# Kernel optimization log

Measured on AMD Instinct MI355X. Metric: run time of the kernel, lower is better.

## Reference

```python
import jax, jax.numpy as jnp
import numpy as np
import math

D_MODEL = 1024
NHEAD = 16
D_K = D_MODEL // NHEAD
NUM_LAYERS = 4
D_FF = 4096
SEQ = 2048
BATCH = 1
EPS = 1e-5


def _layer_norm(x, g, b):
    mu = jnp.mean(x, axis=-1, keepdims=True)
    var = jnp.mean((x - mu) ** 2, axis=-1, keepdims=True)
    return (x - mu) * jax.lax.rsqrt(var + EPS) * g + b


def setup_inputs() -> dict:
    key = jax.random.key(0)
    ks = jax.random.split(key, 16)
    s = 0.02
    L, D, F = NUM_LAYERS, D_MODEL, D_FF
    inp = {
        "x": jax.random.normal(ks[0], (BATCH, SEQ, D), dtype=jnp.float32),
        "wq": jax.random.normal(ks[1], (L, D, D), dtype=jnp.float32) * s,
        "bq": jnp.zeros((L, D), dtype=jnp.float32),
        "wk": jax.random.normal(ks[2], (L, D, D), dtype=jnp.float32) * s,
        "bk": jnp.zeros((L, D), dtype=jnp.float32),
        "wv": jax.random.normal(ks[3], (L, D, D), dtype=jnp.float32) * s,
        "bv": jnp.zeros((L, D), dtype=jnp.float32),
        "wo": jax.random.normal(ks[4], (L, D, D), dtype=jnp.float32) * s,
        "bo": jnp.zeros((L, D), dtype=jnp.float32),
        "w1": jax.random.normal(ks[5], (L, D, F), dtype=jnp.float32) * s,
        "b1": jnp.zeros((L, F), dtype=jnp.float32),
        "w2": jax.random.normal(ks[6], (L, F, D), dtype=jnp.float32) * s,
        "b2": jnp.zeros((L, D), dtype=jnp.float32),
        "ln1_g": jnp.ones((L, D), dtype=jnp.float32),
        "ln1_b": jnp.zeros((L, D), dtype=jnp.float32),
        "ln2_g": jnp.ones((L, D), dtype=jnp.float32),
        "ln2_b": jnp.zeros((L, D), dtype=jnp.float32),
    }
    return inp


def _transformer(x, wq, bq, wk, bk, wv, bv, wo, bo, w1, b1, w2, b2,
                 ln1_g, ln1_b, ln2_g, ln2_b):
    B, S, D = x.shape
    scale = math.sqrt(D_K)
    for l in range(NUM_LAYERS):
        # multi-head self-attention (manual QKV matmul + softmax + matmul)
        q = (x @ wq[l] + bq[l]).reshape(B, S, NHEAD, D_K).transpose(0, 2, 1, 3)
        k = (x @ wk[l] + bk[l]).reshape(B, S, NHEAD, D_K).transpose(0, 2, 1, 3)
        v = (x @ wv[l] + bv[l]).reshape(B, S, NHEAD, D_K).transpose(0, 2, 1, 3)
        scores = jnp.einsum('bhqd,bhkd->bhqk', q, k) / scale  # [B,H,S,S]
        attn = jax.nn.softmax(scores, axis=-1)
        ctx = jnp.einsum('bhqk,bhkd->bhqd', attn, v)
        ctx = ctx.transpose(0, 2, 1, 3).reshape(B, S, D)
        attn_out = ctx @ wo[l] + bo[l]
        x = _layer_norm(x + attn_out, ln1_g[l], ln1_b[l])
        # feed-forward network with gelu
        h = jax.nn.gelu(x @ w1[l] + b1[l])
        ffn_out = h @ w2[l] + b2[l]
        x = _layer_norm(x + ffn_out, ln2_g[l], ln2_b[l])
    return x


def reference(x, wq, bq, wk, bk, wv, bv, wo, bo, w1, b1, w2, b2,
              ln1_g, ln1_b, ln2_g, ln2_b):
    return _transformer(x, wq, bq, wk, bk, wv, bv, wo, bo, w1, b1, w2, b2,
                        ln1_g, ln1_b, ln2_g, ln2_b)
```

## Files before the change

### kernel.cpp

```cpp
#include <hip/hip_runtime.h>
#include <hip/hip_bf16.h>
#include <math.h>

typedef __hip_bfloat16 bf16;
typedef __attribute__((ext_vector_type(8))) short bf16x8;
typedef __attribute__((ext_vector_type(4))) float f32x4;

#define EPI_NONE 0
#define EPI_BIAS_BF16 1
#define EPI_BIAS_GELU_BF16 2

__device__ __forceinline__ void gload16(const void* g, void* l) {
  __builtin_amdgcn_global_load_lds((const __attribute__((address_space(1))) void*)g,
                                   (__attribute__((address_space(3))) void*)l, 16, 0, 0);
}

__device__ __forceinline__ float gelu_tanh(float x) {
  const float c = 0.7978845608028654f;
  float t = tanhf(c * (x + 0.044715f * x * x * x));
  return 0.5f * x * (1.0f + t);
}

template<int BM, int BN, int EPI, typename CT>
__global__ __launch_bounds__(256) void gemm_bt(
    const bf16* __restrict__ A, long sAz, int lda,
    const bf16* __restrict__ Bt, long sBz, int ldb,
    CT* __restrict__ C, long sCz, int ldc,
    const float* __restrict__ bias,
    int K, float scale)
{
  constexpr int BK = 32;
  constexpr int WM = BM / 2, WN = BN / 2;
  constexpr int MI = WM / 16, NJ = WN / 16;
  constexpr int NA = (BM * BK * 2) / 4096;
  constexpr int NB = (BN * BK * 2) / 4096;
  __shared__ __align__(16) bf16 As[BM * BK];
  __shared__ __align__(16) bf16 Bs[BN * BK];
  const int t = threadIdx.x;
  const int lane = t & 63, w = t >> 6;
  const int wm = (w >> 1) * WM, wn = (w & 1) * WN;
  const int quad = lane >> 4, r16 = lane & 15;
  const long z = blockIdx.z;
  const bf16* Ab = A + z * sAz + (long)blockIdx.y * BM * lda;
  const bf16* Bb = Bt + z * sBz + (long)blockIdx.x * BN * ldb;

  f32x4 acc[MI][NJ];
  #pragma unroll
  for (int i = 0; i < MI; ++i)
    #pragma unroll
    for (int j = 0; j < NJ; ++j)
      acc[i][j] = (f32x4){0.f, 0.f, 0.f, 0.f};

  for (int k0 = 0; k0 < K; k0 += BK) {
    __syncthreads();
    #pragma unroll
    for (int s = 0; s < NA; ++s) {
      int Lb = s * 4096 + t * 16;
      int row = Lb >> 6, colb = Lb & 63;
      gload16((const char*)Ab + (long)row * (lda * 2) + k0 * 2 + colb, (char*)As + Lb);
    }
    #pragma unroll
    for (int s = 0; s < NB; ++s) {
      int Lb = s * 4096 + t * 16;
      int row = Lb >> 6, colb = Lb & 63;
      gload16((const char*)Bb + (long)row * (ldb * 2) + k0 * 2 + colb, (char*)Bs + Lb);
    }
    __syncthreads();

    bf16x8 af[MI], bfv[NJ];
    #pragma unroll
    for (int i = 0; i < MI; ++i)
      af[i] = *(const bf16x8*)&As[(wm + i * 16 + r16) * BK + quad * 8];
    #pragma unroll
    for (int j = 0; j < NJ; ++j)
      bfv[j] = *(const bf16x8*)&Bs[(wn + j * 16 + r16) * BK + quad * 8];
    #pragma unroll
    for (int i = 0; i < MI; ++i)
      #pragma unroll
      for (int j = 0; j < NJ; ++j)
        acc[i][j] = __builtin_amdgcn_mfma_f32_16x16x32_bf16(af[i], bfv[j], acc[i][j], 0, 0, 0);
  }

  CT* Cb = C + z * sCz;
  #pragma unroll
  for (int i = 0; i < MI; ++i) {
    #pragma unroll
    for (int j = 0; j < NJ; ++j) {
      int col = blockIdx.x * BN + wn + j * 16 + r16;
      float bvv = 0.f;
      if constexpr (EPI == EPI_BIAS_BF16 || EPI == EPI_BIAS_GELU_BF16)
        bvv = bias[col];
      #pragma unroll
      for (int r = 0; r < 4; ++r) {
        long row = (long)blockIdx.y * BM + wm + i * 16 + quad * 4 + r;
        float val = acc[i][j][r] * scale + bvv;
        if constexpr (EPI == EPI_BIAS_GELU_BF16) val = gelu_tanh(val);
        if constexpr (sizeof(CT) == 2)
          Cb[row * (long)ldc + col] = __float2bfloat16(val);
        else
          Cb[row * (long)ldc + col] = val;
      }
    }
  }
}

__global__ __launch_bounds__(256) void flash_attn(
    const bf16* __restrict__ qkv, const bf16* __restrict__ vT,
    bf16* __restrict__ ctx)
{
  constexpr int SEQ = 2048, LDP = 72;
  __shared__ __align__(16) bf16 Qs[64 * 64];
  __shared__ __align__(16) bf16 Ks[64 * LDP];
  __shared__ __align__(16) bf16 VTs[64 * LDP];
  __shared__ __align__(16) bf16 Ps[64 * LDP];

  const int t = threadIdx.x;
  const int lane = t & 63, w = t >> 6;
  const int quad = lane >> 4, r16 = lane & 15;
  const int wq0 = w * 16;
  const int s0 = blockIdx.x * 64;
  const int h = blockIdx.y;

  #pragma unroll
  for (int s = 0; s < 2; ++s) {
    int Lb = s * 4096 + t * 16;
    int row = Lb >> 7, colb = Lb & 127;
    int4 v = *(const int4*)(qkv + (long)(s0 + row) * 3072 + h * 64 + (colb >> 1));
    *(int4*)((char*)Qs + Lb) = v;
  }

  const bf16* kp[2]; const bf16* vp[2];
  int krow[2], kcolb[2];
  #pragma unroll
  for (int s = 0; s < 2; ++s) {
    int Lb = s * 4096 + t * 16;
    krow[s] = Lb >> 7; kcolb[s] = Lb & 127;
    kp[s] = qkv + 1024 + (long)h * 64 + (long)krow[s] * 3072 + (kcolb[s] >> 1);
    vp[s] = vT + (long)(h * 64 + krow[s]) * SEQ + (kcolb[s] >> 1);
  }

  int4 rk[2], rv[2];
  #pragma unroll
  for (int s = 0; s < 2; ++s) {
    rk[s] = *(const int4*)(kp[s]);
    rv[s] = *(const int4*)(vp[s]);
  }

  __syncthreads();
  bf16x8 af_q[2];
  #pragma unroll
  for (int kk = 0; kk < 2; ++kk)
    af_q[kk] = *(const bf16x8*)&Qs[(wq0 + r16) * 64 + kk * 32 + quad * 8];

  f32x4 O[4];
  float m_s[4], l_s[4];
  #pragma unroll
  for (int jd = 0; jd < 4; ++jd) O[jd] = (f32x4){0.f, 0.f, 0.f, 0.f};
  #pragma unroll
  for (int r = 0; r < 4; ++r) { m_s[r] = -1e30f; l_s[r] = 0.f; }

  for (int kt = 0; kt < SEQ / 64; ++kt) {
    __syncthreads();
    #pragma unroll
    for (int s = 0; s < 2; ++s) {
      *(int4*)((char*)Ks + (krow[s] * LDP * 2) + kcolb[s]) = rk[s];
      *(int4*)((char*)VTs + (krow[s] * LDP * 2) + kcolb[s]) = rv[s];
    }
    __syncthreads();

    if (kt + 1 < SEQ / 64) {
      long k0n = (long)(kt + 1) * 64;
      #pragma unroll
      for (int s = 0; s < 2; ++s) {
        rk[s] = *(const int4*)(kp[s] + k0n * 3072);
        rv[s] = *(const int4*)(vp[s] + k0n);
      }
    }

    f32x4 sc[4];
    #pragma unroll
    for (int j = 0; j < 4; ++j) sc[j] = (f32x4){0.f, 0.f, 0.f, 0.f};
    #pragma unroll
    for (int kk = 0; kk < 2; ++kk) {
      bf16x8 bk_f[4];
      #pragma unroll
      for (int j = 0; j < 4; ++j)
        bk_f[j] = *(const bf16x8*)&Ks[(j * 16 + r16) * LDP + kk * 32 + quad * 8];
      #pragma unroll
      for (int j = 0; j < 4; ++j)
        sc[j] = __builtin_amdgcn_mfma_f32_16x16x32_bf16(af_q[kk], bk_f[j], sc[j], 0, 0, 0);
    }

    #pragma unroll
    for (int r = 0; r < 4; ++r) {
      float mx = -1e30f;
      #pragma unroll
      for (int j = 0; j < 4; ++j) {
        sc[j][r] *= 0.125f;
        mx = fmaxf(mx, sc[j][r]);
      }
      #pragma unroll
      for (int msk = 1; msk < 16; msk <<= 1)
        mx = fmaxf(mx, __shfl_xor(mx, msk));
      float m_new = fmaxf(m_s[r], mx);
      float alpha = __expf(m_s[r] - m_new);
      m_s[r] = m_new;
      float rs = 0.f;
      #pragma unroll
      for (int j = 0; j < 4; ++j) {
        float pv = __expf(sc[j][r] - m_new);
        sc[j][r] = pv;
        rs += pv;
      }
      #pragma unroll
      for (int msk = 1; msk < 16; msk <<= 1)
        rs += __shfl_xor(rs, msk);
      l_s[r] = l_s[r] * alpha + rs;
      #pragma unroll
      for (int jd = 0; jd < 4; ++jd) O[jd][r] *= alpha;
    }

    {
      int prow = wq0 + quad * 4;
      #pragma unroll
      for (int j = 0; j < 4; ++j)
        #pragma unroll
        for (int r = 0; r < 4; ++r)
          Ps[(prow + r) * LDP + j * 16 + r16] = __float2bfloat16(sc[j][r]);
    }
    __syncthreads();

    #pragma unroll
    for (int kk = 0; kk < 2; ++kk) {
      bf16x8 af_p, bv_f[4];
      af_p = *(const bf16x8*)&Ps[(wq0 + r16) * LDP + kk * 32 + quad * 8];
      #pragma unroll
      for (int jd = 0; jd < 4; ++jd)
        bv_f[jd] = *(const bf16x8*)&VTs[(jd * 16 + r16) * LDP + kk * 32 + quad * 8];
      #pragma unroll
      for (int jd = 0; jd < 4; ++jd)
        O[jd] = __builtin_amdgcn_mfma_f32_16x16x32_bf16(af_p, bv_f[jd], O[jd], 0, 0, 0);
    }
  }

  #pragma unroll
  for (int r = 0; r < 4; ++r) {
    long row = s0 + wq0 + quad * 4 + r;
    float inv = 1.f / l_s[r];
    #pragma unroll
    for (int jd = 0; jd < 4; ++jd)
      ctx[row * 1024 + h * 64 + jd * 16 + r16] = __float2bfloat16(O[jd][r] * inv);
  }
}

__global__ __launch_bounds__(256) void transpose_cast(
    const float* __restrict__ in, bf16* __restrict__ out, int R, int C)
{
  __shared__ bf16 tile[32][33];
  const int tx = threadIdx.x, ty = threadIdx.y;
  const int r0 = blockIdx.y * 32, c0 = blockIdx.x * 32;
  #pragma unroll
  for (int d = 0; d < 32; d += 8)
    tile[ty + d][tx] = __float2bfloat16(in[(long)(r0 + ty + d) * C + c0 + tx]);
  __syncthreads();
  #pragma unroll
  for (int d = 0; d < 32; d += 8)
    out[(long)(c0 + ty + d) * R + r0 + tx] = tile[tx][ty + d];
}

__global__ __launch_bounds__(256) void transpose_bf16(
    const bf16* __restrict__ in, bf16* __restrict__ out, int R, int C, int ldin)
{
  __shared__ bf16 tile[32][33];
  const int tx = threadIdx.x, ty = threadIdx.y;
  const int r0 = blockIdx.y * 32, c0 = blockIdx.x * 32;
  #pragma unroll
  for (int d = 0; d < 32; d += 8)
    tile[ty + d][tx] = in[(long)(r0 + ty + d) * ldin + c0 + tx];
  __syncthreads();
  #pragma unroll
  for (int d = 0; d < 32; d += 8)
    out[(long)(c0 + ty + d) * R + r0 + tx] = tile[tx][ty + d];
}

__device__ __forceinline__ float blk_sum(float v, float* sh) {
  #pragma unroll
  for (int o = 32; o > 0; o >>= 1) v += __shfl_down(v, o);
  __syncthreads();
  if ((threadIdx.x & 63) == 0) sh[threadIdx.x >> 6] = v;
  __syncthreads();
  return sh[0] + sh[1] + sh[2] + sh[3];
}

__global__ __launch_bounds__(256) void ln_residual2(
    float* __restrict__ X, const float* __restrict__ d0, const float* __restrict__ d1,
    const float* __restrict__ bias,
    const float* __restrict__ g, const float* __restrict__ b,
    bf16* __restrict__ xb)
{
  __shared__ float sh[4];
  const int t = threadIdx.x;
  const long base = (long)blockIdx.x * 1024;
  float v[4]; float s = 0.f;
  #pragma unroll
  for (int i = 0; i < 4; ++i) {
    int c = t + i * 256;
    float val = X[base + c] + d0[base + c] + d1[base + c] + bias[c];
    v[i] = val; s += val;
  }
  s = blk_sum(s, sh);
  const float mu = s * (1.f / 1024.f);
  float s2 = 0.f;
  #pragma unroll
  for (int i = 0; i < 4; ++i) { float d = v[i] - mu; s2 += d * d; }
  s2 = blk_sum(s2, sh);
  const float rs = rsqrtf(s2 * (1.f / 1024.f) + 1e-5f);
  #pragma unroll
  for (int i = 0; i < 4; ++i) {
    int c = t + i * 256;
    float o = (v[i] - mu) * rs * g[c] + b[c];
    X[base + c] = o;
    xb[base + c] = __float2bfloat16(o);
  }
}

__global__ __launch_bounds__(256) void init_x(
    const float* __restrict__ xin, float* __restrict__ X, bf16* __restrict__ xb, int n)
{
  for (int i = blockIdx.x * 256 + threadIdx.x; i < n; i += gridDim.x * 256) {
    float v = xin[i];
    X[i] = v;
    xb[i] = __float2bfloat16(v);
  }
}

__global__ __launch_bounds__(256) void copy_out(
    const float* __restrict__ X, float* __restrict__ out, int n)
{
  for (int i = blockIdx.x * 256 + threadIdx.x; i < n; i += gridDim.x * 256)
    out[i] = X[i];
}

__global__ __launch_bounds__(256) void concat_bias(
    const float* __restrict__ bq, const float* __restrict__ bk,
    const float* __restrict__ bv, float* __restrict__ out, int n)
{
  for (int i = blockIdx.x * 256 + threadIdx.x; i < n; i += gridDim.x * 256) {
    int l = i / 3072, r = i % 3072;
    int j = r / 1024, c = r % 1024;
    const float* src = (j == 0) ? bq : (j == 1) ? bk : bv;
    out[i] = src[l * 1024 + c];
  }
}

extern "C" void kernel_launch(void* const* d_in, const int* in_sizes, int n_in,
                              void* d_out, int out_size, void* d_ws, size_t ws_size,
                              hipStream_t stream) {
  constexpr int S = 2048, D = 1024, F = 4096, L = 4;
  const float* xin = (const float*)d_in[0];
  const float* wq = (const float*)d_in[1];
  const float* bq = (const float*)d_in[2];
  const float* wk = (const float*)d_in[3];
  const float* bk = (const float*)d_in[4];
  const float* wv = (const float*)d_in[5];
  const float* bvp = (const float*)d_in[6];
  const float* wo = (const float*)d_in[7];
  const float* bo = (const float*)d_in[8];
  const float* w1 = (const float*)d_in[9];
  const float* b1 = (const float*)d_in[10];
  const float* w2 = (const float*)d_in[11];
  const float* b2 = (const float*)d_in[12];
  const float* ln1g = (const float*)d_in[13];
  const float* ln1b = (const float*)d_in[14];
  const float* ln2g = (const float*)d_in[15];
  const float* ln2b = (const float*)d_in[16];

  char* p = (char*)d_ws;
  float* X    = (float*)p; p += (long)S * D * 4;
  float* tmpf = (float*)p; p += 2L * S * D * 4;
  bf16* xb    = (bf16*)p;  p += (long)S * D * 2;
  bf16* qkv   = (bf16*)p;
  bf16* hb    = (bf16*)p;  p += (long)S * 3 * D * 2;
  bf16* ctx   = (bf16*)p;  p += (long)S * D * 2;
  bf16* vT    = (bf16*)p;  p += (long)S * D * 2;
  bf16* wT    = (bf16*)p;  p += (long)F * D * 2;
  float* bias3= (float*)p; p += (long)L * 3 * D * 4;

  init_x<<<2048, 256, 0, stream>>>(xin, X, xb, S * D);
  concat_bias<<<48, 256, 0, stream>>>(bq, bk, bvp, bias3, L * 3 * D);

  for (int l = 0; l < L; ++l) {
    transpose_cast<<<dim3(D / 32, D / 32), dim3(32, 8), 0, stream>>>(wq + (long)l * D * D, wT, D, D);
    transpose_cast<<<dim3(D / 32, D / 32), dim3(32, 8), 0, stream>>>(wk + (long)l * D * D, wT + (long)D * D, D, D);
    transpose_cast<<<dim3(D / 32, D / 32), dim3(32, 8), 0, stream>>>(wv + (long)l * D * D, wT + 2L * D * D, D, D);
    gemm_bt<128, 128, EPI_BIAS_BF16, bf16><<<dim3(3 * D / 128, S / 128, 1), 256, 0, stream>>>(
        xb, 0L, D, wT, 0L, D, qkv, 0L, 3 * D, bias3 + l * 3 * D, D, 1.f);

    transpose_bf16<<<dim3(D / 32, S / 32), dim3(32, 8), 0, stream>>>(qkv + 2 * D, vT, S, D, 3 * D);

    flash_attn<<<dim3(S / 64, 16), 256, 0, stream>>>(qkv, vT, ctx);

    transpose_cast<<<dim3(D / 32, D / 32), dim3(32, 8), 0, stream>>>(wo + (long)l * D * D, wT, D, D);
    gemm_bt<128, 64, EPI_NONE, float><<<dim3(D / 64, S / 128, 2), 256, 0, stream>>>(
        ctx, (long)(D / 2), D, wT, (long)(D / 2), D, tmpf, (long)S * D, D, nullptr, D / 2, 1.f);
    ln_residual2<<<S, 256, 0, stream>>>(X, tmpf, tmpf + (long)S * D, bo + l * D,
                                        ln1g + l * D, ln1b + l * D, xb);

    transpose_cast<<<dim3(F / 32, D / 32), dim3(32, 8), 0, stream>>>(w1 + (long)l * D * F, wT, D, F);
    gemm_bt<128, 128, EPI_BIAS_GELU_BF16, bf16><<<dim3(F / 128, S / 128, 1), 256, 0, stream>>>(
        xb, 0L, D, wT, 0L, D, hb, 0L, F, b1 + l * F, D, 1.f);
    transpose_cast<<<dim3(D / 32, F / 32), dim3(32, 8), 0, stream>>>(w2 + (long)l * F * D, wT, F, D);
    gemm_bt<128, 64, EPI_NONE, float><<<dim3(D / 64, S / 128, 2), 256, 0, stream>>>(
        hb, (long)(F / 2), F, wT, (long)(F / 2), F, tmpf, (long)S * D, D, nullptr, F / 2, 1.f);
    ln_residual2<<<S, 256, 0, stream>>>(X, tmpf, tmpf + (long)S * D, b2 + l * D,
                                        ln2g + l * D, ln2b + l * D, xb);
  }
  copy_out<<<2048, 256, 0, stream>>>(X, (float*)d_out, S * D);
}
```

Baseline: 1.241 ms.

## Split attention over KV halves, use exp2 softmax, and widen GEMM K tile

Flash attention now splits the key range into two halves along a new grid dimension. Each half writes unnormalized fp32 partial outputs plus per-row max and sum, and a new combine kernel merges them into bf16 context. This doubles the attention block count to fill more compute units, at the cost of extra fp32 traffic and one more launch. The softmax folds the 1/8 scale into a log2e constant and uses exp2f. The GEMM K tile is raised from 32 to 64 to halve barriers per K step, at the cost of more LDS per block.

```diff
diff --git a/kernel.cpp b/kernel.cpp
--- a/kernel.cpp
+++ b/kernel.cpp
@@ -9,6 +9,8 @@
 #define EPI_NONE 0
 #define EPI_BIAS_BF16 1
 #define EPI_BIAS_GELU_BF16 2
+
+#define CLOG 0.18033688f
 
 __device__ __forceinline__ void gload16(const void* g, void* l) {
   __builtin_amdgcn_global_load_lds((const __attribute__((address_space(1))) void*)g,
@@ -21,7 +23,7 @@
   return 0.5f * x * (1.0f + t);
 }
 
-template<int BM, int BN, int EPI, typename CT>
+template<int BM, int BN, int BK, int EPI, typename CT>
 __global__ __launch_bounds__(256) void gemm_bt(
     const bf16* __restrict__ A, long sAz, int lda,
     const bf16* __restrict__ Bt, long sBz, int ldb,
@@ -29,11 +31,11 @@
     const float* __restrict__ bias,
     int K, float scale)
 {
-  constexpr int BK = 32;
   constexpr int WM = BM / 2, WN = BN / 2;
   constexpr int MI = WM / 16, NJ = WN / 16;
   constexpr int NA = (BM * BK * 2) / 4096;
   constexpr int NB = (BN * BK * 2) / 4096;
+  constexpr int ROWB = BK * 2;
   __shared__ __align__(16) bf16 As[BM * BK];
   __shared__ __align__(16) bf16 Bs[BN * BK];
   const int t = threadIdx.x;
@@ -56,29 +58,32 @@
     #pragma unroll
     for (int s = 0; s < NA; ++s) {
       int Lb = s * 4096 + t * 16;
-      int row = Lb >> 6, colb = Lb & 63;
+      int row = Lb / ROWB, colb = Lb % ROWB;
       gload16((const char*)Ab + (long)row * (lda * 2) + k0 * 2 + colb, (char*)As + Lb);
     }
     #pragma unroll
     for (int s = 0; s < NB; ++s) {
       int Lb = s * 4096 + t * 16;
-      int row = Lb >> 6, colb = Lb & 63;
+      int row = Lb / ROWB, colb = Lb % ROWB;
       gload16((const char*)Bb + (long)row * (ldb * 2) + k0 * 2 + colb, (char*)Bs + Lb);
     }
     __syncthreads();
 
-    bf16x8 af[MI], bfv[NJ];
-    #pragma unroll
-    for (int i = 0; i < MI; ++i)
-      af[i] = *(const bf16x8*)&As[(wm + i * 16 + r16) * BK + quad * 8];
-    #pragma unroll
-    for (int j = 0; j < NJ; ++j)
-      bfv[j] = *(const bf16x8*)&Bs[(wn + j * 16 + r16) * BK + quad * 8];
-    #pragma unroll
-    for (int i = 0; i < MI; ++i)
+    #pragma unroll
+    for (int kk = 0; kk < BK / 32; ++kk) {
+      bf16x8 af[MI], bfv[NJ];
+      #pragma unroll
+      for (int i = 0; i < MI; ++i)
+        af[i] = *(const bf16x8*)&As[(wm + i * 16 + r16) * BK + kk * 32 + quad * 8];
       #pragma unroll
       for (int j = 0; j < NJ; ++j)
-        acc[i][j] = __builtin_amdgcn_mfma_f32_16x16x32_bf16(af[i], bfv[j], acc[i][j], 0, 0, 0);
+        bfv[j] = *(const bf16x8*)&Bs[(wn + j * 16 + r16) * BK + kk * 32 + quad * 8];
+      #pragma unroll
+      for (int i = 0; i < MI; ++i)
+        #pragma unroll
+        for (int j = 0; j < NJ; ++j)
+          acc[i][j] = __builtin_amdgcn_mfma_f32_16x16x32_bf16(af[i], bfv[j], acc[i][j], 0, 0, 0);
+    }
   }
 
   CT* Cb = C + z * sCz;
@@ -106,7 +111,7 @@
 
 __global__ __launch_bounds__(256) void flash_attn(
     const bf16* __restrict__ qkv, const bf16* __restrict__ vT,
-    bf16* __restrict__ ctx)
+    float* __restrict__ Osp, float2* __restrict__ ml)
 {
   constexpr int SEQ = 2048, LDP = 72;
   __shared__ __align__(16) bf16 Qs[64 * 64];
@@ -120,6 +125,8 @@
   const int wq0 = w * 16;
   const int s0 = blockIdx.x * 64;
   const int h = blockIdx.y;
+  const int split = blockIdx.z;
+  const int kt0 = split * 16, ktN = kt0 + 16;
 
   #pragma unroll
   for (int s = 0; s < 2; ++s) {
@@ -142,8 +149,8 @@
   int4 rk[2], rv[2];
   #pragma unroll
   for (int s = 0; s < 2; ++s) {
-    rk[s] = *(const int4*)(kp[s]);
-    rv[s] = *(const int4*)(vp[s]);
+    rk[s] = *(const int4*)(kp[s] + (long)kt0 * 64 * 3072);
+    rv[s] = *(const int4*)(vp[s] + (long)kt0 * 64);
   }
 
   __syncthreads();
@@ -159,7 +166,7 @@
   #pragma unroll
   for (int r = 0; r < 4; ++r) { m_s[r] = -1e30f; l_s[r] = 0.f; }
 
-  for (int kt = 0; kt < SEQ / 64; ++kt) {
+  for (int kt = kt0; kt < ktN; ++kt) {
     __syncthreads();
     #pragma unroll
     for (int s = 0; s < 2; ++s) {
@@ -168,7 +175,7 @@
     }
     __syncthreads();
 
-    if (kt + 1 < SEQ / 64) {
+    if (kt + 1 < ktN) {
       long k0n = (long)(kt + 1) * 64;
       #pragma unroll
       for (int s = 0; s < 2; ++s) {
@@ -193,22 +200,17 @@
 
     #pragma unroll
     for (int r = 0; r < 4; ++r) {
-      float mx = -1e30f;
-      #pragma unroll
-      for (int j = 0; j < 4; ++j) {
-        sc[j][r] *= 0.125f;
-        mx = fmaxf(mx, sc[j][r]);
-      }
+      float mx = fmaxf(fmaxf(sc[0][r], sc[1][r]), fmaxf(sc[2][r], sc[3][r]));
       #pragma unroll
       for (int msk = 1; msk < 16; msk <<= 1)
         mx = fmaxf(mx, __shfl_xor(mx, msk));
-      float m_new = fmaxf(m_s[r], mx);
-      float alpha = __expf(m_s[r] - m_new);
+      float m_new = fmaxf(m_s[r], mx * CLOG);
+      float alpha = exp2f(m_s[r] - m_new);
       m_s[r] = m_new;
       float rs = 0.f;
       #pragma unroll
       for (int j = 0; j < 4; ++j) {
-        float pv = __expf(sc[j][r] - m_new);
+        float pv = exp2f(fmaf(sc[j][r], CLOG, -m_new));
         sc[j][r] = pv;
         rs += pv;
       }
@@ -243,13 +245,36 @@
     }
   }
 
+  float* Ob = Osp + (long)split * SEQ * 1024;
   #pragma unroll
   for (int r = 0; r < 4; ++r) {
     long row = s0 + wq0 + quad * 4 + r;
-    float inv = 1.f / l_s[r];
     #pragma unroll
     for (int jd = 0; jd < 4; ++jd)
-      ctx[row * 1024 + h * 64 + jd * 16 + r16] = __float2bfloat16(O[jd][r] * inv);
+      Ob[row * 1024 + h * 64 + jd * 16 + r16] = O[jd][r];
+    if (r16 == 0)
+      ml[((long)(split * 16 + h)) * SEQ + row] = make_float2(m_s[r], l_s[r]);
+  }
+}
+
+__global__ __launch_bounds__(256) void attn_combine(
+    const float* __restrict__ Osp, const float2* __restrict__ ml,
+    bf16* __restrict__ ctx)
+{
+  constexpr long SD = 2048L * 1024L;
+  const int s = blockIdx.x;
+  const int t = threadIdx.x;
+  #pragma unroll
+  for (int i = 0; i < 4; ++i) {
+    int c = t + i * 256;
+    int h = c >> 6;
+    float2 a = ml[(long)h * 2048 + s];
+    float2 b = ml[(long)(16 + h) * 2048 + s];
+    float mC = fmaxf(a.x, b.x);
+    float w0 = exp2f(a.x - mC), w1 = exp2f(b.x - mC);
+    float inv = 1.f / (a.y * w0 + b.y * w1);
+    float o = (Osp[(long)s * 1024 + c] * w0 + Osp[SD + (long)s * 1024 + c] * w1) * inv;
+    ctx[(long)s * 1024 + c] = __float2bfloat16(o);
   }
 }
 
@@ -385,6 +410,7 @@
   bf16* vT    = (bf16*)p;  p += (long)S * D * 2;
   bf16* wT    = (bf16*)p;  p += (long)F * D * 2;
   float* bias3= (float*)p; p += (long)L * 3 * D * 4;
+  float2* ml  = (float2*)p; p += 2L * 16 * S * 8;
 
   init_x<<<2048, 256, 0, stream>>>(xin, X, xb, S * D);
   concat_bias<<<48, 256, 0, stream>>>(bq, bk, bvp, bias3, L * 3 * D);
@@ -393,24 +419,25 @@
     transpose_cast<<<dim3(D / 32, D / 32), dim3(32, 8), 0, stream>>>(wq + (long)l * D * D, wT, D, D);
     transpose_cast<<<dim3(D / 32, D / 32), dim3(32, 8), 0, stream>>>(wk + (long)l * D * D, wT + (long)D * D, D, D);
     transpose_cast<<<dim3(D / 32, D / 32), dim3(32, 8), 0, stream>>>(wv + (long)l * D * D, wT + 2L * D * D, D, D);
-    gemm_bt<128, 128, EPI_BIAS_BF16, bf16><<<dim3(3 * D / 128, S / 128, 1), 256, 0, stream>>>(
+    gemm_bt<128, 128, 64, EPI_BIAS_BF16, bf16><<<dim3(3 * D / 128, S / 128, 1), 256, 0, stream>>>(
         xb, 0L, D, wT, 0L, D, qkv, 0L, 3 * D, bias3 + l * 3 * D, D, 1.f);
 
     transpose_bf16<<<dim3(D / 32, S / 32), dim3(32, 8), 0, stream>>>(qkv + 2 * D, vT, S, D, 3 * D);
 
-    flash_attn<<<dim3(S / 64, 16), 256, 0, stream>>>(qkv, vT, ctx);
+    flash_attn<<<dim3(S / 64, 16, 2), 256, 0, stream>>>(qkv, vT, tmpf, ml);
+    attn_combine<<<S, 256, 0, stream>>>(tmpf, ml, ctx);
 
     transpose_cast<<<dim3(D / 32, D / 32), dim3(32, 8), 0, stream>>>(wo + (long)l * D * D, wT, D, D);
-    gemm_bt<128, 64, EPI_NONE, float><<<dim3(D / 64, S / 128, 2), 256, 0, stream>>>(
+    gemm_bt<128, 64, 64, EPI_NONE, float><<<dim3(D / 64, S / 128, 2), 256, 0, stream>>>(
         ctx, (long)(D / 2), D, wT, (long)(D / 2), D, tmpf, (long)S * D, D, nullptr, D / 2, 1.f);
     ln_residual2<<<S, 256, 0, stream>>>(X, tmpf, tmpf + (long)S * D, bo + l * D,
                                         ln1g + l * D, ln1b + l * D, xb);
 
     transpose_cast<<<dim3(F / 32, D / 32), dim3(32, 8), 0, stream>>>(w1 + (long)l * D * F, wT, D, F);
-    gemm_bt<128, 128, EPI_BIAS_GELU_BF16, bf16><<<dim3(F / 128, S / 128, 1), 256, 0, stream>>>(
+    gemm_bt<128, 128, 64, EPI_BIAS_GELU_BF16, bf16><<<dim3(F / 128, S / 128, 1), 256, 0, stream>>>(
         xb, 0L, D, wT, 0L, D, hb, 0L, F, b1 + l * F, D, 1.f);
     transpose_cast<<<dim3(D / 32, F / 32), dim3(32, 8), 0, stream>>>(w2 + (long)l * F * D, wT, F, D);
-    gemm_bt<128, 64, EPI_NONE, float><<<dim3(D / 64, S / 128, 2), 256, 0, stream>>>(
+    gemm_bt<128, 64, 64, EPI_NONE, float><<<dim3(D / 64, S / 128, 2), 256, 0, stream>>>(
         hb, (long)(F / 2), F, wT, (long)(F / 2), F, tmpf, (long)S * D, D, nullptr, F / 2, 1.f);
     ln_residual2<<<S, 256, 0, stream>>>(X, tmpf, tmpf + (long)S * D, b2 + l * D,
                                         ln2g + l * D, ln2b + l * D, xb);
```

Measured after the change: 1.204 ms. 1.03x faster.
